# Kernel tuning notes

Hardware: AMD Instinct MI355X
Metric: run time of the kernel (lower is better)

## Reference

```python
import jax, jax.numpy as jnp
import numpy as np

TAGSET = 64
START_TAG = 62
STOP_TAG = 63
B, S = 32, 256


def setup_inputs() -> dict:
    key = jax.random.key(0)
    k1, k2, k3 = jax.random.split(key, 3)
    features = jax.random.normal(k1, (B, S, TAGSET, TAGSET), dtype=jnp.float32)
    targets = jax.random.randint(k2, (B, S), 0, TAGSET * TAGSET, dtype=jnp.int64)
    lengths = jax.random.randint(k3, (B,), 1, S + 1, dtype=jnp.int64)
    # pack_padded_sequence requires lengths sorted descending; ensure max length = S
    lengths = jnp.sort(lengths)[::-1].at[0].set(S)
    return {"features": features, "targets": targets, "lengths": lengths}


def reference(features, targets, lengths):
    Bc, Sc, T, _ = features.shape
    # --- gold score: gather the score of the true (from_tag, to_tag) pair per token ---
    flat = features.reshape(Bc, Sc, T * T)                       # [B,S,T*T]
    scores_at_targets = jnp.take_along_axis(flat, targets[:, :, None], axis=2)[..., 0]
    valid = (jnp.arange(Sc)[None, :] < lengths[:, None])          # [B,S] pad mask
    gold_score = jnp.sum(jnp.where(valid, scores_at_targets, 0.0))

    # --- CRF forward algorithm (log-sum-exp recurrence over time) ---
    init = features[:, 0, START_TAG, :]                           # [B,T] (all lengths >= 1)
    feats_t = jnp.swapaxes(features, 0, 1)[1:]                    # [S-1,B,T,T]
    active = (jnp.arange(1, Sc)[:, None] < lengths[None, :])       # [S-1,B]

    def step(scores, inp):
        feat, act = inp                                           # feat [B,T,T], act [B]
        new = jax.nn.logsumexp(feat + scores[:, :, None], axis=1)  # lse over from-tag
        scores = jnp.where(act[:, None], new, scores)
        return scores, None

    scores_upto_t, _ = jax.lax.scan(step, init, (feats_t, active))
    all_paths_scores = jnp.sum(scores_upto_t[:, STOP_TAG])

    return (all_paths_scores - gold_score) / Bc
```

## Files before the change

kernel.cpp:

```cpp
#include <hip/hip_runtime.h>
#include <cmath>

#define NB 32
#define NS 256
#define NT 64
#define START_TAG 62
#define STOP_TAG 63
#define CL 8
#define NCH 32
#define GS 8.0f
#define LOG64 4.1588830833596715f
#define CMAT_SHORTS ((size_t)NB * NCH * NT * NT)

typedef __attribute__((ext_vector_type(8))) short short8;
typedef __attribute__((ext_vector_type(4))) float float4v;

union FragU { unsigned u[4]; short8 s; unsigned short h[8]; };

__device__ inline unsigned pkbf(float a, float b) {
  unsigned ua = (__float_as_uint(a) + 0x8000u) >> 16;
  unsigned ub = (__float_as_uint(b) + 0x8000u) & 0xffff0000u;
  return ua | ub;
}

__global__ __launch_bounds__(256) void crf_fused(
    const float* __restrict__ feat, const int* __restrict__ targets,
    const int* __restrict__ lengths, unsigned short* __restrict__ cmat,
    unsigned int* __restrict__ cnt, float* __restrict__ out) {
  const int wv  = threadIdx.x >> 6;
  const int gid = blockIdx.x * 4 + wv;
  const int b   = gid >> 5;
  const int c   = gid & 31;
  const int len = lengths[b];
  const int t1  = 1 + c * CL;
  const int nmat = min(len, t1 + CL) - t1;

  const int lane = threadIdx.x & 63;
  const int q  = lane >> 4;
  const int cc = lane & 15;

  __shared__ float sv[NT];

  if (nmat > 0) {
    const float* fb = feat + ((size_t)b * NS + t1) * (NT * NT);

    FragU BQ[2][4];
    #pragma unroll
    for (int h = 0; h < 2; ++h)
      #pragma unroll
      for (int tj = 0; tj < 4; ++tj) {
        const float* p = fb + (16 * tj + cc) * NT + 32 * h + 8 * q;
        float4 x = *(const float4*)p;
        float4 y = *(const float4*)(p + 4);
        BQ[h][tj].u[0] = pkbf(__expf(x.x - GS), __expf(x.y - GS));
        BQ[h][tj].u[1] = pkbf(__expf(x.z - GS), __expf(x.w - GS));
        BQ[h][tj].u[2] = pkbf(__expf(y.x - GS), __expf(y.y - GS));
        BQ[h][tj].u[3] = pkbf(__expf(y.z - GS), __expf(y.w - GS));
      }

    float raw[4][2][8];
    if (nmat > 1) {
      const float* p = fb + NT * NT;
      #pragma unroll
      for (int mi = 0; mi < 4; ++mi)
        #pragma unroll
        for (int kh = 0; kh < 2; ++kh)
          #pragma unroll
          for (int j = 0; j < 8; ++j)
            raw[mi][kh][j] = p[(32 * kh + 8 * q + j) * NT + 16 * mi + cc];
    }

    const int src0 = (((q & 1) * 2) << 4) | cc;
    const int src1 = src0 + 16;
    const bool hi = (q >> 1) != 0;

    for (int k = 1; k < nmat; ++k) {
      FragU FA[4][2];
      #pragma unroll
      for (int mi = 0; mi < 4; ++mi)
        #pragma unroll
        for (int kh = 0; kh < 2; ++kh)
          #pragma unroll
          for (int j2 = 0; j2 < 4; ++j2)
            FA[mi][kh].u[j2] =
                pkbf(__expf(raw[mi][kh][2 * j2]     - (GS + LOG64)),
                     __expf(raw[mi][kh][2 * j2 + 1] - (GS + LOG64)));

      if (k + 1 < nmat) {
        const float* p = fb + (size_t)(k + 1) * (NT * NT);
        #pragma unroll
        for (int mi = 0; mi < 4; ++mi)
          #pragma unroll
          for (int kh = 0; kh < 2; ++kh)
            #pragma unroll
            for (int j = 0; j < 8; ++j)
              raw[mi][kh][j] = p[(32 * kh + 8 * q + j) * NT + 16 * mi + cc];
      }

      float4v acc[4][4];
      #pragma unroll
      for (int ti = 0; ti < 4; ++ti)
        #pragma unroll
        for (int tj = 0; tj < 4; ++tj) {
          float4v z = {0.f, 0.f, 0.f, 0.f};
          z = __builtin_amdgcn_mfma_f32_16x16x32_bf16(FA[ti][0].s, BQ[0][tj].s, z, 0, 0, 0);
          acc[ti][tj] = __builtin_amdgcn_mfma_f32_16x16x32_bf16(FA[ti][1].s, BQ[1][tj].s, z, 0, 0, 0);
        }

      unsigned pk01[4][4], pk23[4][4];
      #pragma unroll
      for (int ti = 0; ti < 4; ++ti)
        #pragma unroll
        for (int tj = 0; tj < 4; ++tj) {
          pk01[ti][tj] = pkbf(acc[ti][tj][0], acc[ti][tj][1]);
          pk23[ti][tj] = pkbf(acc[ti][tj][2], acc[ti][tj][3]);
        }

      #pragma unroll
      for (int h = 0; h < 2; ++h)
        #pragma unroll
        for (int tj = 0; tj < 4; ++tj) {
          unsigned a0 = (unsigned)__shfl((int)pk01[2 * h][tj],     src0);
          unsigned b0 = (unsigned)__shfl((int)pk01[2 * h + 1][tj], src0);
          unsigned a1 = (unsigned)__shfl((int)pk23[2 * h][tj],     src0);
          unsigned b1 = (unsigned)__shfl((int)pk23[2 * h + 1][tj], src0);
          unsigned a2 = (unsigned)__shfl((int)pk01[2 * h][tj],     src1);
          unsigned b2 = (unsigned)__shfl((int)pk01[2 * h + 1][tj], src1);
          unsigned a3 = (unsigned)__shfl((int)pk23[2 * h][tj],     src1);
          unsigned b3 = (unsigned)__shfl((int)pk23[2 * h + 1][tj], src1);
          BQ[h][tj].u[0] = hi ? b0 : a0;
          BQ[h][tj].u[1] = hi ? b1 : a1;
          BQ[h][tj].u[2] = hi ? b2 : a2;
          BQ[h][tj].u[3] = hi ? b3 : a3;
        }
    }

    unsigned short* dst = cmat + ((size_t)b * NCH + c) * (NT * NT);
    #pragma unroll
    for (int h = 0; h < 2; ++h)
      #pragma unroll
      for (int tj = 0; tj < 4; ++tj)
        #pragma unroll
        for (int j = 0; j < 8; ++j)
          dst[(32 * h + 8 * q + j) * NT + 16 * tj + cc] = BQ[h][tj].h[j];
  }

  __threadfence();
  unsigned old = 0;
  if (lane == 0) old = atomicAdd(&cnt[b], 1u);
  old = (unsigned)__shfl((int)old, 0);
  if (old != NCH - 1) return;
  __threadfence();

  const int j = lane;
  const float* f0 = feat + (size_t)b * NS * (NT * NT);

  float gold = 0.f;
  #pragma unroll
  for (int g = 0; g < 4; ++g) {
    const int s = j + 64 * g;
    if (s < len) {
      const int tgt = targets[b * NS + s];
      gold += f0[(size_t)s * (NT * NT) + tgt];
    }
  }

  float x = f0[START_TAG * NT + j];
  float m = x;
  #pragma unroll
  for (int off = 32; off; off >>= 1) m = fmaxf(m, __shfl_xor(m, off));
  float v = __expf(x - m);
  float L = m;

  const int nch = (len - 1 + CL - 1) / CL;
  const uint4* base = (const uint4*)(cmat + (size_t)b * NCH * (NT * NT)) + j * 8;

  uint4 QA[8], QB[8], QC[8];
  auto LQ = [&](uint4* D, int c2) {
    if (c2 < nch) {
      const uint4* P = base + (size_t)c2 * 512;
      #pragma unroll
      for (int w = 0; w < 8; ++w) D[w] = P[w];
    }
  };
  auto STEP = [&](const uint4* Q, int c2) {
    sv[j] = v;
    __builtin_amdgcn_wave_barrier();
    float ac0 = 0.f, ac1 = 0.f, ac2 = 0.f, ac3 = 0.f;
    const float4* svp = (const float4*)sv;
    #pragma unroll
    for (int w = 0; w < 8; ++w) {
      uint4 qq = Q[w];
      float4 s0 = svp[2 * w], s1 = svp[2 * w + 1];
      ac0 = fmaf(__uint_as_float(qq.x << 16), s0.x, ac0);
      ac1 = fmaf(__uint_as_float(qq.x & 0xffff0000u), s0.y, ac1);
      ac2 = fmaf(__uint_as_float(qq.y << 16), s0.z, ac2);
      ac3 = fmaf(__uint_as_float(qq.y & 0xffff0000u), s0.w, ac3);
      ac0 = fmaf(__uint_as_float(qq.z << 16), s1.x, ac0);
      ac1 = fmaf(__uint_as_float(qq.z & 0xffff0000u), s1.y, ac1);
      ac2 = fmaf(__uint_as_float(qq.w << 16), s1.z, ac2);
      ac3 = fmaf(__uint_as_float(qq.w & 0xffff0000u), s1.w, ac3);
    }
    float acc = (ac0 + ac1) + (ac2 + ac3);
    __builtin_amdgcn_wave_barrier();
    const int tt1 = 1 + c2 * CL;
    const int nm = min(len, tt1 + CL) - tt1;
    L += (float)nm * GS + (float)(nm - 1) * LOG64;
    float mm = acc;
    #pragma unroll
    for (int off = 32; off; off >>= 1) mm = fmaxf(mm, __shfl_xor(mm, off));
    v = acc / mm;
    L += __logf(mm);
  };

  LQ(QA, 0); LQ(QB, 1); LQ(QC, 2);
  for (int c2 = 0; c2 < nch; c2 += 3) {
    STEP(QA, c2);
    LQ(QA, c2 + 3);
    if (c2 + 1 < nch) { STEP(QB, c2 + 1); LQ(QB, c2 + 4); }
    if (c2 + 2 < nch) { STEP(QC, c2 + 2); LQ(QC, c2 + 5); }
  }

  float lv = __logf(v);
  float path = L + __shfl(lv, STOP_TAG);

  #pragma unroll
  for (int off = 32; off; off >>= 1) gold += __shfl_down(gold, off);
  if (j == 0) atomicAdd(out, (path - gold) * (1.0f / (float)NB));
}

extern "C" void kernel_launch(void* const* d_in, const int* in_sizes, int n_in,
                              void* d_out, int out_size, void* d_ws, size_t ws_size,
                              hipStream_t stream) {
  const float* feat    = (const float*)d_in[0];
  const int*   targets = (const int*)d_in[1];
  const int*   lengths = (const int*)d_in[2];
  unsigned short* cmat = (unsigned short*)d_ws;
  unsigned int* cnt = (unsigned int*)((char*)d_ws + CMAT_SHORTS * 2);
  float* out = (float*)d_out;

  hipMemsetAsync(cnt, 0, NB * sizeof(unsigned int), stream);
  hipMemsetAsync(d_out, 0, sizeof(float), stream);
  crf_fused<<<NB * NCH / 4, 256, 0, stream>>>(feat, targets, lengths, cmat, cnt, out);
}
```

Measured before the change: 260.7 us.

## Split fused CRF kernel into chunk and combine kernels, drop memsets

Replaces the single fused kernel, which used a per-batch atomic counter and threadfence so the last-finishing wave ran the sequential combine, with two launches: a chunk-product kernel and a per-batch combine kernel. The output zeroing moves into the first kernel, removing both hipMemsetAsync calls. This drops the two memset launches, the fences and the atomics, and the early-exit waves no longer hold the combine path. In exchange it adds a kernel boundary and gives up the overlap where combines could start while other batches' chunks were still running.

```diff
diff --git a/kernel.cpp b/kernel.cpp
--- a/kernel.cpp
+++ b/kernel.cpp
@@ -10,7 +10,6 @@
 #define NCH 32
 #define GS 8.0f
 #define LOG64 4.1588830833596715f
-#define CMAT_SHORTS ((size_t)NB * NCH * NT * NT)
 
 typedef __attribute__((ext_vector_type(8))) short short8;
 typedef __attribute__((ext_vector_type(4))) float float4v;
@@ -23,10 +22,11 @@
   return ua | ub;
 }
 
-__global__ __launch_bounds__(256) void crf_fused(
-    const float* __restrict__ feat, const int* __restrict__ targets,
-    const int* __restrict__ lengths, unsigned short* __restrict__ cmat,
-    unsigned int* __restrict__ cnt, float* __restrict__ out) {
+__global__ __launch_bounds__(256) void chunk_kernel(
+    const float* __restrict__ feat, const int* __restrict__ lengths,
+    unsigned short* __restrict__ cmat, float* __restrict__ out) {
+  if (blockIdx.x == 0 && threadIdx.x == 0) out[0] = 0.f;
+
   const int wv  = threadIdx.x >> 6;
   const int gid = blockIdx.x * 4 + wv;
   const int b   = gid >> 5;
@@ -34,33 +34,58 @@
   const int len = lengths[b];
   const int t1  = 1 + c * CL;
   const int nmat = min(len, t1 + CL) - t1;
+  if (nmat <= 0) return;
 
   const int lane = threadIdx.x & 63;
   const int q  = lane >> 4;
   const int cc = lane & 15;
 
-  __shared__ float sv[NT];
-
-  if (nmat > 0) {
-    const float* fb = feat + ((size_t)b * NS + t1) * (NT * NT);
-
-    FragU BQ[2][4];
-    #pragma unroll
-    for (int h = 0; h < 2; ++h)
-      #pragma unroll
-      for (int tj = 0; tj < 4; ++tj) {
-        const float* p = fb + (16 * tj + cc) * NT + 32 * h + 8 * q;
-        float4 x = *(const float4*)p;
-        float4 y = *(const float4*)(p + 4);
-        BQ[h][tj].u[0] = pkbf(__expf(x.x - GS), __expf(x.y - GS));
-        BQ[h][tj].u[1] = pkbf(__expf(x.z - GS), __expf(x.w - GS));
-        BQ[h][tj].u[2] = pkbf(__expf(y.x - GS), __expf(y.y - GS));
-        BQ[h][tj].u[3] = pkbf(__expf(y.z - GS), __expf(y.w - GS));
-      }
-
-    float raw[4][2][8];
-    if (nmat > 1) {
-      const float* p = fb + NT * NT;
+  const float* fb = feat + ((size_t)b * NS + t1) * (NT * NT);
+
+  FragU BQ[2][4];
+  #pragma unroll
+  for (int h = 0; h < 2; ++h)
+    #pragma unroll
+    for (int tj = 0; tj < 4; ++tj) {
+      const float* p = fb + (16 * tj + cc) * NT + 32 * h + 8 * q;
+      float4 x = *(const float4*)p;
+      float4 y = *(const float4*)(p + 4);
+      BQ[h][tj].u[0] = pkbf(__expf(x.x - GS), __expf(x.y - GS));
+      BQ[h][tj].u[1] = pkbf(__expf(x.z - GS), __expf(x.w - GS));
+      BQ[h][tj].u[2] = pkbf(__expf(y.x - GS), __expf(y.y - GS));
+      BQ[h][tj].u[3] = pkbf(__expf(y.z - GS), __expf(y.w - GS));
+    }
+
+  float raw[4][2][8];
+  if (nmat > 1) {
+    const float* p = fb + NT * NT;
+    #pragma unroll
+    for (int mi = 0; mi < 4; ++mi)
+      #pragma unroll
+      for (int kh = 0; kh < 2; ++kh)
+        #pragma unroll
+        for (int j = 0; j < 8; ++j)
+          raw[mi][kh][j] = p[(32 * kh + 8 * q + j) * NT + 16 * mi + cc];
+  }
+
+  const int src0 = (((q & 1) * 2) << 4) | cc;
+  const int src1 = src0 + 16;
+  const bool hi = (q >> 1) != 0;
+
+  for (int k = 1; k < nmat; ++k) {
+    FragU FA[4][2];
+    #pragma unroll
+    for (int mi = 0; mi < 4; ++mi)
+      #pragma unroll
+      for (int kh = 0; kh < 2; ++kh)
+        #pragma unroll
+        for (int j2 = 0; j2 < 4; ++j2)
+          FA[mi][kh].u[j2] =
+              pkbf(__expf(raw[mi][kh][2 * j2]     - (GS + LOG64)),
+                   __expf(raw[mi][kh][2 * j2 + 1] - (GS + LOG64)));
+
+    if (k + 1 < nmat) {
+      const float* p = fb + (size_t)(k + 1) * (NT * NT);
       #pragma unroll
       for (int mi = 0; mi < 4; ++mi)
         #pragma unroll
@@ -70,89 +95,62 @@
             raw[mi][kh][j] = p[(32 * kh + 8 * q + j) * NT + 16 * mi + cc];
     }
 
-    const int src0 = (((q & 1) * 2) << 4) | cc;
-    const int src1 = src0 + 16;
-    const bool hi = (q >> 1) != 0;
-
-    for (int k = 1; k < nmat; ++k) {
-      FragU FA[4][2];
-      #pragma unroll
-      for (int mi = 0; mi < 4; ++mi)
-        #pragma unroll
-        for (int kh = 0; kh < 2; ++kh)
-          #pragma unroll
-          for (int j2 = 0; j2 < 4; ++j2)
-            FA[mi][kh].u[j2] =
-                pkbf(__expf(raw[mi][kh][2 * j2]     - (GS + LOG64)),
-                     __expf(raw[mi][kh][2 * j2 + 1] - (GS + LOG64)));
-
-      if (k + 1 < nmat) {
-        const float* p = fb + (size_t)(k + 1) * (NT * NT);
-        #pragma unroll
-        for (int mi = 0; mi < 4; ++mi)
-          #pragma unroll
-          for (int kh = 0; kh < 2; ++kh)
-            #pragma unroll
-            for (int j = 0; j < 8; ++j)
-              raw[mi][kh][j] = p[(32 * kh + 8 * q + j) * NT + 16 * mi + cc];
+    float4v acc[4][4];
+    #pragma unroll
+    for (int ti = 0; ti < 4; ++ti)
+      #pragma unroll
+      for (int tj = 0; tj < 4; ++tj) {
+        float4v z = {0.f, 0.f, 0.f, 0.f};
+        z = __builtin_amdgcn_mfma_f32_16x16x32_bf16(FA[ti][0].s, BQ[0][tj].s, z, 0, 0, 0);
+        acc[ti][tj] = __builtin_amdgcn_mfma_f32_16x16x32_bf16(FA[ti][1].s, BQ[1][tj].s, z, 0, 0, 0);
       }
 
-      float4v acc[4][4];
-      #pragma unroll
-      for (int ti = 0; ti < 4; ++ti)
-        #pragma unroll
-        for (int tj = 0; tj < 4; ++tj) {
-          float4v z = {0.f, 0.f, 0.f, 0.f};
-          z = __builtin_amdgcn_mfma_f32_16x16x32_bf16(FA[ti][0].s, BQ[0][tj].s, z, 0, 0, 0);
-          acc[ti][tj] = __builtin_amdgcn_mfma_f32_16x16x32_bf16(FA[ti][1].s, BQ[1][tj].s, z, 0, 0, 0);
-        }
-
-      unsigned pk01[4][4], pk23[4][4];
-      #pragma unroll
-      for (int ti = 0; ti < 4; ++ti)
-        #pragma unroll
-        for (int tj = 0; tj < 4; ++tj) {
-          pk01[ti][tj] = pkbf(acc[ti][tj][0], acc[ti][tj][1]);
-          pk23[ti][tj] = pkbf(acc[ti][tj][2], acc[ti][tj][3]);
-        }
-
-      #pragma unroll
-      for (int h = 0; h < 2; ++h)
-        #pragma unroll
-        for (int tj = 0; tj < 4; ++tj) {
-          unsigned a0 = (unsigned)__shfl((int)pk01[2 * h][tj],     src0);
-          unsigned b0 = (unsigned)__shfl((int)pk01[2 * h + 1][tj], src0);
-          unsigned a1 = (unsigned)__shfl((int)pk23[2 * h][tj],     src0);
-          unsigned b1 = (unsigned)__shfl((int)pk23[2 * h + 1][tj], src0);
-          unsigned a2 = (unsigned)__shfl((int)pk01[2 * h][tj],     src1);
-          unsigned b2 = (unsigned)__shfl((int)pk01[2 * h + 1][tj], src1);
-          unsigned a3 = (unsigned)__shfl((int)pk23[2 * h][tj],     src1);
-          unsigned b3 = (unsigned)__shfl((int)pk23[2 * h + 1][tj], src1);
-          BQ[h][tj].u[0] = hi ? b0 : a0;
-          BQ[h][tj].u[1] = hi ? b1 : a1;
-          BQ[h][tj].u[2] = hi ? b2 : a2;
-          BQ[h][tj].u[3] = hi ? b3 : a3;
-        }
-    }
-
-    unsigned short* dst = cmat + ((size_t)b * NCH + c) * (NT * NT);
+    unsigned pk01[4][4], pk23[4][4];
+    #pragma unroll
+    for (int ti = 0; ti < 4; ++ti)
+      #pragma unroll
+      for (int tj = 0; tj < 4; ++tj) {
+        pk01[ti][tj] = pkbf(acc[ti][tj][0], acc[ti][tj][1]);
+        pk23[ti][tj] = pkbf(acc[ti][tj][2], acc[ti][tj][3]);
+      }
+
     #pragma unroll
     for (int h = 0; h < 2; ++h)
       #pragma unroll
-      for (int tj = 0; tj < 4; ++tj)
-        #pragma unroll
-        for (int j = 0; j < 8; ++j)
-          dst[(32 * h + 8 * q + j) * NT + 16 * tj + cc] = BQ[h][tj].h[j];
-  }
-
-  __threadfence();
-  unsigned old = 0;
-  if (lane == 0) old = atomicAdd(&cnt[b], 1u);
-  old = (unsigned)__shfl((int)old, 0);
-  if (old != NCH - 1) return;
-  __threadfence();
-
-  const int j = lane;
+      for (int tj = 0; tj < 4; ++tj) {
+        unsigned a0 = (unsigned)__shfl((int)pk01[2 * h][tj],     src0);
+        unsigned b0 = (unsigned)__shfl((int)pk01[2 * h + 1][tj], src0);
+        unsigned a1 = (unsigned)__shfl((int)pk23[2 * h][tj],     src0);
+        unsigned b1 = (unsigned)__shfl((int)pk23[2 * h + 1][tj], src0);
+        unsigned a2 = (unsigned)__shfl((int)pk01[2 * h][tj],     src1);
+        unsigned b2 = (unsigned)__shfl((int)pk01[2 * h + 1][tj], src1);
+        unsigned a3 = (unsigned)__shfl((int)pk23[2 * h][tj],     src1);
+        unsigned b3 = (unsigned)__shfl((int)pk23[2 * h + 1][tj], src1);
+        BQ[h][tj].u[0] = hi ? b0 : a0;
+        BQ[h][tj].u[1] = hi ? b1 : a1;
+        BQ[h][tj].u[2] = hi ? b2 : a2;
+        BQ[h][tj].u[3] = hi ? b3 : a3;
+      }
+  }
+
+  unsigned short* dst = cmat + ((size_t)b * NCH + c) * (NT * NT);
+  #pragma unroll
+  for (int h = 0; h < 2; ++h)
+    #pragma unroll
+    for (int tj = 0; tj < 4; ++tj)
+      #pragma unroll
+      for (int j = 0; j < 8; ++j)
+        dst[(32 * h + 8 * q + j) * NT + 16 * tj + cc] = BQ[h][tj].h[j];
+}
+
+__global__ __launch_bounds__(64) void combine_kernel(
+    const float* __restrict__ feat, const int* __restrict__ targets,
+    const int* __restrict__ lengths, const unsigned int* __restrict__ cmat,
+    float* __restrict__ out) {
+  const int b = blockIdx.x;
+  const int j = threadIdx.x;
+  __shared__ float sv[NT];
+  const int len = lengths[b];
   const float* f0 = feat + (size_t)b * NS * (NT * NT);
 
   float gold = 0.f;
@@ -173,7 +171,7 @@
   float L = m;
 
   const int nch = (len - 1 + CL - 1) / CL;
-  const uint4* base = (const uint4*)(cmat + (size_t)b * NCH * (NT * NT)) + j * 8;
+  const uint4* base = (const uint4*)cmat + (size_t)b * NCH * 512 + j * 8;
 
   uint4 QA[8], QB[8], QC[8];
   auto LQ = [&](uint4* D, int c2) {
@@ -236,10 +234,9 @@
   const int*   targets = (const int*)d_in[1];
   const int*   lengths = (const int*)d_in[2];
   unsigned short* cmat = (unsigned short*)d_ws;
-  unsigned int* cnt = (unsigned int*)((char*)d_ws + CMAT_SHORTS * 2);
   float* out = (float*)d_out;
 
-  hipMemsetAsync(cnt, 0, NB * sizeof(unsigned int), stream);
-  hipMemsetAsync(d_out, 0, sizeof(float), stream);
-  crf_fused<<<NB * NCH / 4, 256, 0, stream>>>(feat, targets, lengths, cmat, cnt, out);
-}
+  chunk_kernel<<<NB * NCH / 4, 256, 0, stream>>>(feat, lengths, cmat, out);
+  combine_kernel<<<NB, 64, 0, stream>>>(feat, targets, lengths,
+                                        (const unsigned int*)cmat, out);
+}
```

After: 213.2 us. -18.2%, faster.
